# Kernel tuning notes

Hardware: AMD Instinct MI355X
Metric: run time of the kernel (lower is better)

Reference implementation:

```python
import jax, jax.numpy as jnp
import numpy as np

R_CHK, N_VAR, BATCH, ITERS, NLEV, ROW_DEG = 144, 576, 512, 3, 16, 15


def setup_inputs() -> dict:
    key = jax.random.key(0)
    rng = np.random.default_rng(0)
    Hnp = np.zeros((R_CHK, N_VAR), np.float32)
    cols = np.argsort(rng.random((R_CHK, N_VAR)), axis=1)[:, :ROW_DEG]
    Hnp[np.arange(R_CHK)[:, None], cols] = 1.0
    H = jnp.asarray(Hnp)
    r = jax.random.normal(key, (BATCH, N_VAR), jnp.float32) * 2.0  # channel LLRs
    alpha = jnp.full((ITERS,), 0.7, jnp.float32)
    beta = jnp.full((ITERS,), 0.05, jnp.float32)
    eta = jnp.full((ITERS,), 0.7, jnp.float32)
    qk = jnp.linspace(-4.0, 4.0, NLEV).astype(jnp.float32)  # learned codebook
    return {"r": r, "alpha": alpha, "beta": beta, "eta": eta, "qk": qk, "H": H}


def _c_to_v(M, alpha, beta, Hb):
    # Normalized offset min-sum check-node update, excluding self-message.
    mag = jnp.where(Hb, jnp.abs(M), jnp.inf)              # [B,R,C]
    two = -jax.lax.top_k(-mag, 2)[0]                      # two smallest per row
    m1, m2 = two[..., 0:1], two[..., 1:2]
    min_excl = jnp.where(mag == m1, m2, m1)               # min over other edges
    sgn = jnp.where(Hb, jnp.sign(M), 1.0)
    row_sign = jnp.prod(sgn, axis=-1, keepdims=True)
    E = alpha * row_sign * sgn * jnp.maximum(min_excl - beta, 0.0)
    return jnp.where(Hb, E, 0.0)


def _quantize(x, eta, qk):
    # Nearest-level lookup in sorted codebook qk, applied to eta*x.
    bnd = 0.5 * (qk[:-1] + qk[1:])                        # [NLEV-1] midpoints
    idx = jnp.searchsorted(bnd, eta * x)
    return qk[idx]


def _decode(r, alpha, beta, eta, qk, H):
    Hb = H > 0.5                                          # [R,C] edge mask
    M = H[None] * r[:, None, :]                           # initial_M: [B,R,C]
    E = jnp.zeros_like(M)
    for it in range(ITERS):
        E = _c_to_v(M, alpha[it], beta[it], Hb)
        E = _quantize(E, eta[it], qk) * H                 # Q on check messages
        col = jnp.sum(E, axis=1, keepdims=True)           # [B,1,C]
        M = H[None] * (r[:, None, :] + col - E)           # update_M (extrinsic)
        M = _quantize(M, eta[it], qk) * H                 # Q on var messages
    return r + jnp.sum(E, axis=1)                         # [B,C]


def reference(r, alpha, beta, eta, qk, H):
    return _decode(r, alpha, beta, eta, qk, H)
```

## Files before the change

### kernel.cpp

```cpp
#include <hip/hip_runtime.h>
#include <hip/hip_bf16.h>
#include <math.h>

#define R_CHK   144
#define N_VAR   576
#define BATCH   512
#define ITERS   3
#define NLEV    16
#define ROW_DEG 15
#define N_EDGE  (R_CHK * ROW_DEG)
#define NWORDS  9

__launch_bounds__(64)
__global__ void k1_bitmask(const float* __restrict__ H,
                           unsigned long long* __restrict__ bits,
                           int* __restrict__ edge_cols) {
    const int i    = blockIdx.x;
    const int lane = threadIdx.x;

    float h[NWORDS];
#pragma unroll
    for (int s = 0; s < NWORDS; ++s) h[s] = H[i * N_VAR + s * 64 + lane];

    unsigned long long m[NWORDS];
#pragma unroll
    for (int s = 0; s < NWORDS; ++s) m[s] = __ballot(h[s] > 0.5f);

#pragma unroll
    for (int s = 0; s < NWORDS; ++s)
        if (lane == s) bits[i * NWORDS + s] = m[s];

    if (lane == 0) {
        int k = 0;
#pragma unroll
        for (int s = 0; s < NWORDS; ++s) {
            unsigned long long mm = m[s];
            while (mm) {
                int b = __ffsll((long long)mm) - 1;
                if (k < ROW_DEG) edge_cols[i * ROW_DEG + k] = s * 64 + b;
                ++k;
                mm &= mm - 1;
            }
        }
    }
}

__launch_bounds__(N_VAR)
__global__ void k2_csr(const unsigned long long* __restrict__ bits,
                       int* __restrict__ col_ptr,
                       int* __restrict__ col_csr) {
    __shared__ unsigned long long sb[R_CHK * NWORDS];
    __shared__ int spref[R_CHK * NWORDS];
    __shared__ int sscan[2][N_VAR];

    const int t = threadIdx.x;

    for (int e = t; e < R_CHK * NWORDS; e += N_VAR) sb[e] = bits[e];
    __syncthreads();

    for (int idx = t; idx < R_CHK * NWORDS; idx += N_VAR) {
        int i = idx / NWORDS, w = idx % NWORDS;
        int p = 0;
        for (int u = 0; u < w; ++u) p += __popcll(sb[i * NWORDS + u]);
        spref[idx] = p;
    }

    const int w   = t >> 6;
    const int bit = t & 63;
    const unsigned long long vmask   = 1ull << bit;
    const unsigned long long lowmask = vmask - 1ull;
    int n = 0;
    for (int i0 = 0; i0 < R_CHK; i0 += 16) {
        unsigned long long mw[16];
#pragma unroll
        for (int j = 0; j < 16; ++j) mw[j] = sb[(i0 + j) * NWORDS + w];
#pragma unroll
        for (int j = 0; j < 16; ++j) n += (int)((mw[j] >> bit) & 1ull);
    }
    __syncthreads();
    sscan[0][t] = n;
    __syncthreads();

    int src = 0;
    for (int off = 1; off < N_VAR; off <<= 1) {
        int v = sscan[src][t];
        if (t >= off) v += sscan[src][t - off];
        sscan[src ^ 1][t] = v;
        src ^= 1;
        __syncthreads();
    }

    const int myptr = sscan[src][t] - n;
    col_ptr[t] = myptr;
    if (t == N_VAR - 1) col_ptr[N_VAR] = sscan[src][t];

    int p = myptr;
    for (int i0 = 0; i0 < R_CHK; i0 += 16) {
        unsigned long long mw[16];
        int pf[16];
#pragma unroll
        for (int j = 0; j < 16; ++j) {
            mw[j] = sb[(i0 + j) * NWORDS + w];
            pf[j] = spref[(i0 + j) * NWORDS + w];
        }
#pragma unroll
        for (int j = 0; j < 16; ++j) {
            if (mw[j] & vmask) {
                int rank = pf[j] + __popcll(mw[j] & lowmask);
                col_csr[p++] = (i0 + j) * ROW_DEG + rank;
            }
        }
    }
}

__launch_bounds__(256)
__global__ void decode_kernel(const float* __restrict__ r,
                              const float* __restrict__ alpha,
                              const float* __restrict__ beta,
                              const float* __restrict__ eta,
                              const float* __restrict__ qk,
                              const int* __restrict__ edge_cols,
                              const int* __restrict__ col_ptr,
                              const int* __restrict__ col_csr,
                              float* __restrict__ out) {
    __shared__ float sE[N_EDGE];
    __shared__ float sr[N_VAR];
    __shared__ float st[N_VAR];
    __shared__ int   s_csr[N_EDGE];
    __shared__ int   s_ptr[N_VAR + 1];

    const int b = blockIdx.x;
    const int t = threadIdx.x;

    const float qv = qk[t & 15];
    float bnd[NLEV - 1];
#pragma unroll
    for (int j = 0; j < NLEV - 1; ++j) bnd[j] = 0.5f * (qk[j] + qk[j + 1]);

    float av[ITERS], bv[ITERS], ev[ITERS];
#pragma unroll
    for (int i = 0; i < ITERS; ++i) { av[i] = alpha[i]; bv[i] = beta[i]; ev[i] = eta[i]; }

    for (int e = t; e < N_EDGE; e += 256) s_csr[e] = col_csr[e];
    for (int v = t; v < N_VAR + 1; v += 256) s_ptr[v] = col_ptr[v];
    for (int v = t; v < N_VAR; v += 256) sr[v] = r[b * N_VAR + v];

    const bool isrow = (t < R_CHK);
    int cols[ROW_DEG];
    if (isrow) {
#pragma unroll
        for (int k = 0; k < ROW_DEG; ++k) cols[k] = edge_cols[t * ROW_DEG + k];
    }
    __syncthreads();

    float M[ROW_DEG], Eq[ROW_DEG];
    if (isrow) {
#pragma unroll
        for (int k = 0; k < ROW_DEG; ++k) M[k] = sr[cols[k]];
    }

#pragma unroll
    for (int it = 0; it < ITERS; ++it) {
        const float a   = av[it];
        const float bta = bv[it];
        const float et  = ev[it];

        if (isrow) {
            if (it > 0) {
                const float etp = ev[it - 1];
#pragma unroll
                for (int k = 0; k < ROW_DEG; ++k) {
                    float x = st[cols[k]] - Eq[k];
                    float y = etp * x;
                    int idx = 0;
#pragma unroll
                    for (int j = 0; j < NLEV - 1; ++j) idx += (y > bnd[j]) ? 1 : 0;
                    M[k] = __shfl(qv, idx);
                }
            }

            float m1 = INFINITY, m2 = INFINITY;
            float prod = 1.0f;
#pragma unroll
            for (int k = 0; k < ROW_DEG; ++k) {
                float ab = fabsf(M[k]);
                if (ab < m1)      { m2 = m1; m1 = ab; }
                else if (ab < m2) { m2 = ab; }
                float s = (M[k] > 0.0f) ? 1.0f : ((M[k] < 0.0f) ? -1.0f : 0.0f);
                prod *= s;
            }
#pragma unroll
            for (int k = 0; k < ROW_DEG; ++k) {
                float ab = fabsf(M[k]);
                float mexcl = (ab == m1) ? m2 : m1;
                float s  = (M[k] > 0.0f) ? 1.0f : ((M[k] < 0.0f) ? -1.0f : 0.0f);
                float E  = ((a * prod) * s) * fmaxf(mexcl - bta, 0.0f);
                float y = et * E;
                int idx = 0;
#pragma unroll
                for (int j = 0; j < NLEV - 1; ++j) idx += (y > bnd[j]) ? 1 : 0;
                float eq = __shfl(qv, idx);
                Eq[k] = eq;
                sE[t * ROW_DEG + k] = eq;
            }
        }
        __syncthreads();

        for (int v = t; v < N_VAR; v += 256) {
            float sum = 0.0f;
            const int p0 = s_ptr[v], p1 = s_ptr[v + 1];
            for (int j = p0; j < p1; ++j) sum += sE[s_csr[j]];
            float stv = sr[v] + sum;
            st[v] = stv;
            if (it == ITERS - 1) out[b * N_VAR + v] = stv;
        }
        if (it < ITERS - 1) __syncthreads();
    }
}

extern "C" void kernel_launch(void* const* d_in, const int* in_sizes, int n_in,
                              void* d_out, int out_size, void* d_ws, size_t ws_size,
                              hipStream_t stream) {
    const float* r     = (const float*)d_in[0];
    const float* alpha = (const float*)d_in[1];
    const float* beta  = (const float*)d_in[2];
    const float* eta   = (const float*)d_in[3];
    const float* qk    = (const float*)d_in[4];
    const float* H     = (const float*)d_in[5];
    float* out = (float*)d_out;

    unsigned long long* bits = (unsigned long long*)d_ws;
    int* edge_cols = (int*)(bits + R_CHK * NWORDS);
    int* col_ptr   = edge_cols + N_EDGE;
    int* col_csr   = col_ptr + (N_VAR + 1);

    k1_bitmask<<<R_CHK, 64, 0, stream>>>(H, bits, edge_cols);
    k2_csr<<<1, N_VAR, 0, stream>>>(bits, col_ptr, col_csr);
    decode_kernel<<<BATCH, 256, 0, stream>>>(r, alpha, beta, eta, qk,
                                             edge_cols, col_ptr, col_csr, out);
}
```

Before: 50.86 us.

## Replace CSR column gather with padded per-variable edge table in registers

The variable-node sum used a CSR (col_ptr/col_csr) built by a prefix scan and staged in shared memory. It now uses a fixed 16-slot edge list per variable, held in registers. Empty slots point at a zero sentinel in sE, so each column sum is a fully unrolled loop with no bounds or pointer loads, and the scan in the setup kernel goes away. The check-node two-minimum search and sign product are also rewritten as pairwise trees to shorten dependency chains. The cost is many more shared-memory reads per variable, since average column degree is about 4 but every variable does 16 reads. The 48 index registers per thread also raise register pressure, and columns with degree above 16 would be silently truncated.

```diff
diff --git a/kernel.cpp b/kernel.cpp
--- a/kernel.cpp
+++ b/kernel.cpp
@@ -10,6 +10,7 @@
 #define ROW_DEG 15
 #define N_EDGE  (R_CHK * ROW_DEG)
 #define NWORDS  9
+#define DEG_PAD 16
 
 __launch_bounds__(64)
 __global__ void k1_bitmask(const float* __restrict__ H,
@@ -46,12 +47,10 @@
 }
 
 __launch_bounds__(N_VAR)
-__global__ void k2_csr(const unsigned long long* __restrict__ bits,
-                       int* __restrict__ col_ptr,
-                       int* __restrict__ col_csr) {
+__global__ void k2_coltab(const unsigned long long* __restrict__ bits,
+                          int* __restrict__ col_edge) {
     __shared__ unsigned long long sb[R_CHK * NWORDS];
     __shared__ int spref[R_CHK * NWORDS];
-    __shared__ int sscan[2][N_VAR];
 
     const int t = threadIdx.x;
 
@@ -64,6 +63,7 @@
         for (int u = 0; u < w; ++u) p += __popcll(sb[i * NWORDS + u]);
         spref[idx] = p;
     }
+    __syncthreads();
 
     const int w   = t >> 6;
     const int bit = t & 63;
@@ -72,31 +72,6 @@
     int n = 0;
     for (int i0 = 0; i0 < R_CHK; i0 += 16) {
         unsigned long long mw[16];
-#pragma unroll
-        for (int j = 0; j < 16; ++j) mw[j] = sb[(i0 + j) * NWORDS + w];
-#pragma unroll
-        for (int j = 0; j < 16; ++j) n += (int)((mw[j] >> bit) & 1ull);
-    }
-    __syncthreads();
-    sscan[0][t] = n;
-    __syncthreads();
-
-    int src = 0;
-    for (int off = 1; off < N_VAR; off <<= 1) {
-        int v = sscan[src][t];
-        if (t >= off) v += sscan[src][t - off];
-        sscan[src ^ 1][t] = v;
-        src ^= 1;
-        __syncthreads();
-    }
-
-    const int myptr = sscan[src][t] - n;
-    col_ptr[t] = myptr;
-    if (t == N_VAR - 1) col_ptr[N_VAR] = sscan[src][t];
-
-    int p = myptr;
-    for (int i0 = 0; i0 < R_CHK; i0 += 16) {
-        unsigned long long mw[16];
         int pf[16];
 #pragma unroll
         for (int j = 0; j < 16; ++j) {
@@ -107,10 +82,12 @@
         for (int j = 0; j < 16; ++j) {
             if (mw[j] & vmask) {
                 int rank = pf[j] + __popcll(mw[j] & lowmask);
-                col_csr[p++] = (i0 + j) * ROW_DEG + rank;
-            }
-        }
-    }
+                if (n < DEG_PAD) col_edge[t * DEG_PAD + n] = (i0 + j) * ROW_DEG + rank;
+                ++n;
+            }
+        }
+    }
+    for (int j = n; j < DEG_PAD; ++j) col_edge[t * DEG_PAD + j] = N_EDGE;
 }
 
 __launch_bounds__(256)
@@ -120,14 +97,11 @@
                               const float* __restrict__ eta,
                               const float* __restrict__ qk,
                               const int* __restrict__ edge_cols,
-                              const int* __restrict__ col_ptr,
-                              const int* __restrict__ col_csr,
+                              const int* __restrict__ col_edge,
                               float* __restrict__ out) {
-    __shared__ float sE[N_EDGE];
+    __shared__ float sE[N_EDGE + 1];
     __shared__ float sr[N_VAR];
     __shared__ float st[N_VAR];
-    __shared__ int   s_csr[N_EDGE];
-    __shared__ int   s_ptr[N_VAR + 1];
 
     const int b = blockIdx.x;
     const int t = threadIdx.x;
@@ -141,9 +115,15 @@
 #pragma unroll
     for (int i = 0; i < ITERS; ++i) { av[i] = alpha[i]; bv[i] = beta[i]; ev[i] = eta[i]; }
 
-    for (int e = t; e < N_EDGE; e += 256) s_csr[e] = col_csr[e];
-    for (int v = t; v < N_VAR + 1; v += 256) s_ptr[v] = col_ptr[v];
-    for (int v = t; v < N_VAR; v += 256) sr[v] = r[b * N_VAR + v];
+    int ce0[DEG_PAD], ce1[DEG_PAD], ce2[DEG_PAD];
+#pragma unroll
+    for (int j = 0; j < DEG_PAD; ++j) ce0[j] = col_edge[t * DEG_PAD + j];
+#pragma unroll
+    for (int j = 0; j < DEG_PAD; ++j) ce1[j] = col_edge[(t + 256) * DEG_PAD + j];
+    if (t < N_VAR - 512) {
+#pragma unroll
+        for (int j = 0; j < DEG_PAD; ++j) ce2[j] = col_edge[(t + 512) * DEG_PAD + j];
+    }
 
     const bool isrow = (t < R_CHK);
     int cols[ROW_DEG];
@@ -151,6 +131,9 @@
 #pragma unroll
         for (int k = 0; k < ROW_DEG; ++k) cols[k] = edge_cols[t * ROW_DEG + k];
     }
+
+    for (int v = t; v < N_VAR; v += 256) sr[v] = r[b * N_VAR + v];
+    if (t == 0) sE[N_EDGE] = 0.0f;
     __syncthreads();
 
     float M[ROW_DEG], Eq[ROW_DEG];
@@ -179,22 +162,43 @@
                 }
             }
 
-            float m1 = INFINITY, m2 = INFINITY;
-            float prod = 1.0f;
-#pragma unroll
-            for (int k = 0; k < ROW_DEG; ++k) {
-                float ab = fabsf(M[k]);
-                if (ab < m1)      { m2 = m1; m1 = ab; }
-                else if (ab < m2) { m2 = ab; }
-                float s = (M[k] > 0.0f) ? 1.0f : ((M[k] < 0.0f) ? -1.0f : 0.0f);
-                prod *= s;
-            }
+            float sg[ROW_DEG];
+#pragma unroll
+            for (int k = 0; k < ROW_DEG; ++k)
+                sg[k] = (M[k] > 0.0f) ? 1.0f : ((M[k] < 0.0f) ? -1.0f : 0.0f);
+            float q0 = sg[0] * sg[1],  q1 = sg[2] * sg[3];
+            float q2 = sg[4] * sg[5],  q3 = sg[6] * sg[7];
+            float q4 = sg[8] * sg[9],  q5 = sg[10] * sg[11];
+            float q6 = sg[12] * sg[13], q7 = sg[14];
+            float r0 = q0 * q1, r1 = q2 * q3, r2 = q4 * q5, r3 = q6 * q7;
+            const float prod = (r0 * r1) * (r2 * r3);
+
+            float a1[8], a2[8];
+#pragma unroll
+            for (int k = 0; k < 7; ++k) {
+                float x = fabsf(M[2 * k]), y = fabsf(M[2 * k + 1]);
+                a1[k] = fminf(x, y); a2[k] = fmaxf(x, y);
+            }
+            a1[7] = fabsf(M[14]); a2[7] = INFINITY;
+#pragma unroll
+            for (int s = 4; s >= 1; s >>= 1) {
+#pragma unroll
+                for (int k = 0; k < 4; ++k) {
+                    if (k < s) {
+                        float lo = fminf(a1[k], a1[k + s]);
+                        float hi = fminf(fmaxf(a1[k], a1[k + s]), fminf(a2[k], a2[k + s]));
+                        a1[k] = lo; a2[k] = hi;
+                    }
+                }
+            }
+            const float m1 = a1[0], m2 = a2[0];
+
+            const float ap = a * prod;
 #pragma unroll
             for (int k = 0; k < ROW_DEG; ++k) {
                 float ab = fabsf(M[k]);
                 float mexcl = (ab == m1) ? m2 : m1;
-                float s  = (M[k] > 0.0f) ? 1.0f : ((M[k] < 0.0f) ? -1.0f : 0.0f);
-                float E  = ((a * prod) * s) * fmaxf(mexcl - bta, 0.0f);
+                float E = (ap * sg[k]) * fmaxf(mexcl - bta, 0.0f);
                 float y = et * E;
                 int idx = 0;
 #pragma unroll
@@ -206,13 +210,30 @@
         }
         __syncthreads();
 
-        for (int v = t; v < N_VAR; v += 256) {
-            float sum = 0.0f;
-            const int p0 = s_ptr[v], p1 = s_ptr[v + 1];
-            for (int j = p0; j < p1; ++j) sum += sE[s_csr[j]];
-            float stv = sr[v] + sum;
-            st[v] = stv;
-            if (it == ITERS - 1) out[b * N_VAR + v] = stv;
+        {
+            float s0 = 0.0f, s1 = 0.0f, s2 = 0.0f;
+#pragma unroll
+            for (int j = 0; j < DEG_PAD; ++j) s0 += sE[ce0[j]];
+#pragma unroll
+            for (int j = 0; j < DEG_PAD; ++j) s1 += sE[ce1[j]];
+            if (t < N_VAR - 512) {
+#pragma unroll
+                for (int j = 0; j < DEG_PAD; ++j) s2 += sE[ce2[j]];
+            }
+            float t0 = sr[t] + s0;
+            float t1 = sr[t + 256] + s1;
+            st[t] = t0;
+            st[t + 256] = t1;
+            float t2 = 0.0f;
+            if (t < N_VAR - 512) {
+                t2 = sr[t + 512] + s2;
+                st[t + 512] = t2;
+            }
+            if (it == ITERS - 1) {
+                out[b * N_VAR + t] = t0;
+                out[b * N_VAR + t + 256] = t1;
+                if (t < N_VAR - 512) out[b * N_VAR + t + 512] = t2;
+            }
         }
         if (it < ITERS - 1) __syncthreads();
     }
@@ -231,11 +252,10 @@
 
     unsigned long long* bits = (unsigned long long*)d_ws;
     int* edge_cols = (int*)(bits + R_CHK * NWORDS);
-    int* col_ptr   = edge_cols + N_EDGE;
-    int* col_csr   = col_ptr + (N_VAR + 1);
+    int* col_edge  = edge_cols + N_EDGE;
 
     k1_bitmask<<<R_CHK, 64, 0, stream>>>(H, bits, edge_cols);
-    k2_csr<<<1, N_VAR, 0, stream>>>(bits, col_ptr, col_csr);
+    k2_coltab<<<1, N_VAR, 0, stream>>>(bits, col_edge);
     decode_kernel<<<BATCH, 256, 0, stream>>>(r, alpha, beta, eta, qk,
-                                             edge_cols, col_ptr, col_csr, out);
-}
+                                             edge_cols, col_edge, out);
+}
```

After: 42.97 us. -15.5%, faster.
